# Kernel optimization log

Measured on AMD Instinct MI355X. Metric: run time of the kernel, lower is better.

Reference implementation:

```python
import jax, jax.numpy as jnp
import numpy as np

B, C, H, W = 8, 256, 128, 128
NW = 512  # n_weights (depthwise multiplier 2)
EPS = 1e-5
SPARSITY = 0.5


def setup_inputs() -> dict:
    key = jax.random.key(0)
    k_x, k_sign, k_mask, k_w1 = jax.random.split(key, 4)
    x = jax.random.normal(k_x, (B, C, H, W), dtype=jnp.float32)
    gamma = jnp.ones((C,), dtype=jnp.float32)
    beta = jnp.zeros((C,), dtype=jnp.float32)
    # frozen binary/sparse LBP depthwise weights in {-1, 0, +1}
    sign = jax.random.bernoulli(k_sign, 0.5, (NW, 1, 3, 3)).astype(jnp.float32) * 2.0 - 1.0
    inactive = jax.random.uniform(k_mask, (NW, 1, 3, 3)) > SPARSITY
    lbp_w = jnp.where(inactive, 0.0, sign)
    # 1x1 conv params (PyTorch default init scale)
    bound = 1.0 / np.sqrt(NW)
    w1 = jax.random.uniform(k_w1, (C, NW, 1, 1), minval=-bound, maxval=bound, dtype=jnp.float32)
    b1 = jnp.zeros((C,), dtype=jnp.float32)
    return {"x": x, "gamma": gamma, "beta": beta, "lbp_w": lbp_w, "w1": w1, "b1": b1}


def reference(x, gamma, beta, lbp_w, w1, b1):
    # BatchNorm2d in training mode: biased batch stats over (N, H, W)
    mean = jnp.mean(x, axis=(0, 2, 3), keepdims=True)
    var = jnp.var(x, axis=(0, 2, 3), keepdims=True)
    xn = (x - mean) * jax.lax.rsqrt(var + EPS)
    xn = xn * gamma[None, :, None, None] + beta[None, :, None, None]
    # depthwise 3x3 conv, padding=1, groups=C (depth multiplier NW//C)
    y = jax.lax.conv_general_dilated(
        xn, lbp_w, window_strides=(1, 1), padding=((1, 1), (1, 1)),
        dimension_numbers=("NCHW", "OIHW", "NCHW"), feature_group_count=C)
    y = jax.nn.relu(y)
    # 1x1 conv NW -> C plus bias, then residual add
    z = jax.lax.conv_general_dilated(
        y, w1, window_strides=(1, 1), padding=((0, 0), (0, 0)),
        dimension_numbers=("NCHW", "OIHW", "NCHW"))
    z = z + b1[None, :, None, None]
    return z + x
```

## Files before the change

### kernel.cpp

```cpp
#include <hip/hip_runtime.h>

#define B_ 8
#define C_ 256
#define H_ 128
#define W_ 128
#define NW_ 512
#define HW_ (H_*W_)
#define EPS_ 1e-5f

typedef __attribute__((ext_vector_type(8))) short bf16x8;
typedef __attribute__((ext_vector_type(4))) float f32x4;

__device__ __forceinline__ unsigned short f2bf(float f) {
  unsigned u = __float_as_uint(f);
  u += 0x7fffu + ((u >> 16) & 1u);
  return (unsigned short)(u >> 16);
}
__device__ __forceinline__ float bf2f(unsigned short h) {
  return __uint_as_float(((unsigned)h) << 16);
}
__device__ __forceinline__ float bflo(unsigned u) { return __uint_as_float(u << 16); }
__device__ __forceinline__ float bfhi(unsigned u) { return __uint_as_float(u & 0xffff0000u); }

__global__ __launch_bounds__(256)
void bn_partial(const float* __restrict__ x, float* __restrict__ psum,
                float* __restrict__ psq) {
  const int b = blockIdx.x, c = blockIdx.y, tid = threadIdx.x;
  const float4* p = (const float4*)(x + (size_t)(b*C_ + c) * HW_);
  float s = 0.f, s2 = 0.f;
  #pragma unroll
  for (int i = 0; i < 16; ++i) {
    float4 v = p[tid + i*256];
    s  += v.x + v.y + v.z + v.w;
    s2 += v.x*v.x + v.y*v.y + v.z*v.z + v.w*v.w;
  }
  #pragma unroll
  for (int off = 32; off > 0; off >>= 1) {
    s  += __shfl_down(s, off);
    s2 += __shfl_down(s2, off);
  }
  __shared__ float rs[4], rq[4];
  if ((tid & 63) == 0) { rs[tid >> 6] = s; rq[tid >> 6] = s2; }
  __syncthreads();
  if (tid == 0) {
    float S = rs[0]+rs[1]+rs[2]+rs[3], S2 = rq[0]+rq[1]+rq[2]+rq[3];
    psum[c*B_ + b] = S;
    psq [c*B_ + b] = S2;
  }
}

__global__ __launch_bounds__(256)
void bn_final(float* __restrict__ wsf, const float* __restrict__ gamma,
              const float* __restrict__ beta) {
  const int c = threadIdx.x;
  float S = 0.f, S2 = 0.f;
  #pragma unroll
  for (int b = 0; b < B_; ++b) { S += wsf[512 + c*B_ + b]; S2 += wsf[2560 + c*B_ + b]; }
  const float n = (float)(B_*HW_);
  float mean = S / n;
  float var  = S2 / n - mean*mean;
  float scl  = gamma[c] * rsqrtf(var + EPS_);
  wsf[c]       = scl;
  wsf[C_ + c]  = beta[c] - mean*scl;
}

__global__ __launch_bounds__(64)
void w1prep(const float* __restrict__ w1, ushort* __restrict__ w1f) {
  const int l15 = threadIdx.x & 15, quad = threadIdx.x >> 4;
  const int mtG = blockIdx.x >> 4, ks = blockIdx.x & 15;
  const float* src = w1 + (size_t)(mtG*16 + l15)*NW_ + ks*32 + quad*8;
  float4 f0 = *(const float4*)src, f1 = *(const float4*)(src + 4);
  union { unsigned u[4]; uint4 q; } cv;
  cv.u[0] = (unsigned)f2bf(f0.x) | ((unsigned)f2bf(f0.y) << 16);
  cv.u[1] = (unsigned)f2bf(f0.z) | ((unsigned)f2bf(f0.w) << 16);
  cv.u[2] = (unsigned)f2bf(f1.x) | ((unsigned)f2bf(f1.y) << 16);
  cv.u[3] = (unsigned)f2bf(f1.z) | ((unsigned)f2bf(f1.w) << 16);
  ((uint4*)w1f)[blockIdx.x*64 + threadIdx.x] = cv.q;
}

template<bool PREW1>
__global__ __launch_bounds__(256, 2)
void fused_mfma(const float* __restrict__ x, const float* __restrict__ lbpw,
                const float* __restrict__ w1raw, const ushort* __restrict__ w1f,
                const float* __restrict__ b1, const float* __restrict__ sc_sh,
                float* __restrict__ out) {
  const int tid  = threadIdx.x;
  const int b    = blockIdx.z;
  const int h0   = blockIdx.y * 4;
  const int w0   = blockIdx.x * 16;
  const int wave = tid >> 6;
  const int lane = tid & 63;
  const int l15  = lane & 15;
  const int quad = lane >> 4;

  __shared__ float  s_scale[C_];
  __shared__ float  s_shift[C_];
  __shared__ float  s_b1[C_];
  __shared__ __align__(16) float  s_xn[16][6][20];
  __shared__ __align__(16) ushort s_yT[64][40];
  __shared__ __align__(16) ushort s_wc[32][16];
  __shared__ __align__(16) ushort s_res[256][66];

  s_scale[tid] = sc_sh[tid];
  s_shift[tid] = sc_sh[C_ + tid];
  s_b1[tid]    = b1[tid];

  const int ccin = tid >> 4;
  const int ccol = tid & 15;

  f32x4 acc[4][4];
  #pragma unroll
  for (int mt = 0; mt < 4; ++mt)
    #pragma unroll
    for (int nt = 0; nt < 4; ++nt) {
      f32x4 z = {0.f, 0.f, 0.f, 0.f};
      acc[mt][nt] = z;
    }

  __syncthreads();

  #pragma unroll 1
  for (int kc = 0; kc < 16; ++kc) {
    const int c0 = kc * 16;
    const int o0 = kc * 32;

    for (int idx = tid; idx < 16*6*18; idx += 256) {
      const int cl  = idx / 108;
      const int rem = idx - cl * 108;
      const int r   = rem / 18;
      const int col = rem - r * 18;
      const int h = h0 + r - 1;
      const int w = w0 + col - 1;
      float v = 0.f;
      if (h >= 0 && h < H_ && w >= 0 && w < W_) {
        const float xv = x[((size_t)(b*C_ + c0 + cl)*H_ + h)*W_ + w];
        v = fmaf(xv, s_scale[c0 + cl], s_shift[c0 + cl]);
        if (r >= 1 && r <= 4 && col >= 1 && col <= 16)
          s_res[c0 + cl][(r-1)*16 + (col-1)] = f2bf(xv);
      }
      s_xn[cl][r][col] = v;
    }
    for (int idx = tid; idx < 32*9; idx += 256) {
      const int oo = idx / 9;
      const int j  = idx - oo * 9;
      s_wc[oo][j] = f2bf(lbpw[(size_t)(o0 + oo)*9 + j]);
    }
    __syncthreads();

    {
      float v[6][3];
      #pragma unroll
      for (int rr = 0; rr < 6; ++rr)
        #pragma unroll
        for (int dj = 0; dj < 3; ++dj)
          v[rr][dj] = s_xn[ccin][rr][ccol + dj];

      const uint4 qa = *(const uint4*)&s_wc[2*ccin][0];
      const uint4 qb = *(const uint4*)&s_wc[2*ccin + 1][0];
      const float wA[9] = { bflo(qa.x), bfhi(qa.x), bflo(qa.y), bfhi(qa.y),
                            bflo(qa.z), bfhi(qa.z), bflo(qa.w), bfhi(qa.w),
                            bf2f(s_wc[2*ccin][8]) };
      const float wB[9] = { bflo(qb.x), bfhi(qb.x), bflo(qb.y), bfhi(qb.y),
                            bflo(qb.z), bfhi(qb.z), bflo(qb.w), bfhi(qb.w),
                            bf2f(s_wc[2*ccin + 1][8]) };
      float a0[4] = {0.f,0.f,0.f,0.f}, a1[4] = {0.f,0.f,0.f,0.f};
      #pragma unroll
      for (int r = 0; r < 4; ++r)
        #pragma unroll
        for (int di = 0; di < 3; ++di)
          #pragma unroll
          for (int dj = 0; dj < 3; ++dj) {
            const float t = v[r + di][dj];
            a0[r] = fmaf(wA[di*3 + dj], t, a0[r]);
            a1[r] = fmaf(wB[di*3 + dj], t, a1[r]);
          }
      #pragma unroll
      for (int r = 0; r < 4; ++r) {
        const unsigned pk = (unsigned)f2bf(fmaxf(a0[r], 0.f)) |
                            ((unsigned)f2bf(fmaxf(a1[r], 0.f)) << 16);
        *(unsigned*)&s_yT[r*16 + ccol][2*ccin] = pk;
      }
    }
    __syncthreads();

    bf16x8 bfr[4];
    #pragma unroll
    for (int nt = 0; nt < 4; ++nt)
      bfr[nt] = *(const bf16x8*)&s_yT[nt*16 + l15][quad*8];

    #pragma unroll
    for (int mt = 0; mt < 4; ++mt) {
      bf16x8 afr;
      if constexpr (PREW1) {
        union { uint4 q; bf16x8 v; } cv;
        cv.q = *(const uint4*)(w1f + (size_t)(((wave*4 + mt)*16 + kc)*64 + lane)*8);
        afr = cv.v;
      } else {
        const float* wp = w1raw + (size_t)(wave*64 + mt*16 + l15)*NW_ + o0 + quad*8;
        const float4 f0 = *(const float4*)wp;
        const float4 f1 = *(const float4*)(wp + 4);
        union { unsigned u[4]; bf16x8 v; } cv;
        cv.u[0] = (unsigned)f2bf(f0.x) | ((unsigned)f2bf(f0.y) << 16);
        cv.u[1] = (unsigned)f2bf(f0.z) | ((unsigned)f2bf(f0.w) << 16);
        cv.u[2] = (unsigned)f2bf(f1.x) | ((unsigned)f2bf(f1.y) << 16);
        cv.u[3] = (unsigned)f2bf(f1.z) | ((unsigned)f2bf(f1.w) << 16);
        afr = cv.v;
      }
      #pragma unroll
      for (int nt = 0; nt < 4; ++nt)
        acc[mt][nt] = __builtin_amdgcn_mfma_f32_16x16x32_bf16(afr, bfr[nt], acc[mt][nt], 0, 0, 0);
    }
    __syncthreads();
  }

  #pragma unroll
  for (int mt = 0; mt < 4; ++mt) {
    #pragma unroll
    for (int nt = 0; nt < 4; ++nt) {
      const int h   = h0 + nt;
      const int wcl = w0 + l15;
      const int px  = nt*16 + l15;
      #pragma unroll
      for (int i = 0; i < 4; ++i) {
        const int ch = wave*64 + mt*16 + quad*4 + i;
        const float r = bf2f(s_res[ch][px]);
        out[((size_t)(b*C_ + ch)*H_ + h)*W_ + wcl] = acc[mt][nt][i] + s_b1[ch] + r;
      }
    }
  }
}

extern "C" void kernel_launch(void* const* d_in, const int* in_sizes, int n_in,
                              void* d_out, int out_size, void* d_ws, size_t ws_size,
                              hipStream_t stream) {
  const float* x     = (const float*)d_in[0];
  const float* gamma = (const float*)d_in[1];
  const float* beta  = (const float*)d_in[2];
  const float* lbpw  = (const float*)d_in[3];
  const float* w1    = (const float*)d_in[4];
  const float* b1    = (const float*)d_in[5];
  float* out = (float*)d_out;

  float* wsf = (float*)d_ws;
  ushort* w1f = (ushort*)((char*)d_ws + 18432);
  const bool pre = ws_size >= (size_t)(18432 + 262144);

  bn_partial<<<dim3(B_, C_), 256, 0, stream>>>(x, wsf + 512, wsf + 2560);
  bn_final<<<1, 256, 0, stream>>>(wsf, gamma, beta);

  dim3 grid(W_/16, H_/4, B_);
  if (pre) {
    w1prep<<<256, 64, 0, stream>>>(w1, w1f);
    fused_mfma<true><<<grid, 256, 0, stream>>>(x, lbpw, w1, w1f, b1, wsf, out);
  } else {
    fused_mfma<false><<<grid, 256, 0, stream>>>(x, lbpw, w1, w1f, b1, wsf, out);
  }
}
```

Baseline: 447.5 us.

## Double-buffer LDS staging, precompute gather geometry, drop residual LDS cache

Double-buffers the normalized input tile, LBP weights and depthwise output in LDS so the next channel chunk's gather is issued before the barrier that precedes the MFMA stage, removing one barrier per iteration. Gather addresses and padding masks are computed once per thread, and pad zeros are written once for both buffers. The residual now comes from a global re-read of x in the epilogue instead of a large bf16 LDS array, which cuts LDS use enough to request 4 blocks per SM. This also makes the residual full fp32, at the cost of extra global traffic and tighter register limits.

```diff
diff --git a/kernel.cpp b/kernel.cpp
--- a/kernel.cpp
+++ b/kernel.cpp
@@ -79,7 +79,7 @@
 }
 
 template<bool PREW1>
-__global__ __launch_bounds__(256, 2)
+__global__ __launch_bounds__(256, 4)
 void fused_mfma(const float* __restrict__ x, const float* __restrict__ lbpw,
                 const float* __restrict__ w1raw, const ushort* __restrict__ w1f,
                 const float* __restrict__ b1, const float* __restrict__ sc_sh,
@@ -92,60 +92,75 @@
   const int lane = tid & 63;
   const int l15  = lane & 15;
   const int quad = lane >> 4;
+  const int cl   = tid >> 4;
+  const int jj   = tid & 15;
 
   __shared__ float  s_scale[C_];
   __shared__ float  s_shift[C_];
   __shared__ float  s_b1[C_];
-  __shared__ __align__(16) float  s_xn[16][6][20];
-  __shared__ __align__(16) ushort s_yT[64][40];
-  __shared__ __align__(16) ushort s_wc[32][16];
-  __shared__ __align__(16) ushort s_res[256][66];
+  __shared__ __align__(16) float  s_xn[2][16][6][20];
+  __shared__ __align__(16) ushort s_yT[2][64][40];
+  __shared__ __align__(16) ushort s_wc[2][32][16];
 
   s_scale[tid] = sc_sh[tid];
   s_shift[tid] = sc_sh[C_ + tid];
   s_b1[tid]    = b1[tid];
 
-  const int ccin = tid >> 4;
-  const int ccol = tid & 15;
-
-  f32x4 acc[4][4];
-  #pragma unroll
-  for (int mt = 0; mt < 4; ++mt)
-    #pragma unroll
-    for (int nt = 0; nt < 4; ++nt) {
-      f32x4 z = {0.f, 0.f, 0.f, 0.f};
-      acc[mt][nt] = z;
-    }
-
-  __syncthreads();
-
-  #pragma unroll 1
-  for (int kc = 0; kc < 16; ++kc) {
-    const int c0 = kc * 16;
-    const int o0 = kc * 32;
-
-    for (int idx = tid; idx < 16*6*18; idx += 256) {
-      const int cl  = idx / 108;
-      const int rem = idx - cl * 108;
-      const int r   = rem / 18;
-      const int col = rem - r * 18;
+  int geo[7];
+  unsigned actmask = 0, padmask = 0;
+  #pragma unroll
+  for (int k = 0; k < 7; ++k) {
+    geo[k] = 0;
+    const int e = jj + 16*k;
+    if (e < 108) {
+      const int r   = e / 18;
+      const int col = e - r*18;
+      const int lofs = cl*120 + r*20 + col;
       const int h = h0 + r - 1;
       const int w = w0 + col - 1;
-      float v = 0.f;
       if (h >= 0 && h < H_ && w >= 0 && w < W_) {
-        const float xv = x[((size_t)(b*C_ + c0 + cl)*H_ + h)*W_ + w];
-        v = fmaf(xv, s_scale[c0 + cl], s_shift[c0 + cl]);
-        if (r >= 1 && r <= 4 && col >= 1 && col <= 16)
-          s_res[c0 + cl][(r-1)*16 + (col-1)] = f2bf(xv);
-      }
-      s_xn[cl][r][col] = v;
-    }
-    for (int idx = tid; idx < 32*9; idx += 256) {
-      const int oo = idx / 9;
-      const int j  = idx - oo * 9;
-      s_wc[oo][j] = f2bf(lbpw[(size_t)(o0 + oo)*9 + j]);
-    }
-    __syncthreads();
+        actmask |= (1u << k);
+        geo[k] = ((cl*HW_ + h*W_ + w) << 11) | lofs;
+      } else {
+        padmask |= (1u << k);
+        geo[k] = lofs;
+      }
+    }
+  }
+  {
+    float* p0 = &s_xn[0][0][0][0];
+    float* p1 = &s_xn[1][0][0][0];
+    #pragma unroll
+    for (int k = 0; k < 7; ++k)
+      if (padmask & (1u << k)) { p0[geo[k] & 2047] = 0.f; p1[geo[k] & 2047] = 0.f; }
+  }
+  const int woA = tid / 9,         wjA = tid - woA*9;
+  const int woB = (tid + 256) / 9, wjB = (tid + 256) - woB*9;
+
+  f32x4 acc[4][4];
+  #pragma unroll
+  for (int mt = 0; mt < 4; ++mt)
+    #pragma unroll
+    for (int nt = 0; nt < 4; ++nt) { f32x4 z = {0.f,0.f,0.f,0.f}; acc[mt][nt] = z; }
+
+  __syncthreads();
+
+  {
+    const float scl = s_scale[cl];
+    const float sh  = s_shift[cl];
+    const float* xc = x + (size_t)(b*C_) * HW_;
+    float* xb = &s_xn[0][0][0][0];
+    #pragma unroll
+    for (int k = 0; k < 7; ++k)
+      if (actmask & (1u << k)) xb[geo[k] & 2047] = fmaf(xc[geo[k] >> 11], scl, sh);
+    s_wc[0][woA][wjA] = f2bf(lbpw[woA*9 + wjA]);
+    if (tid < 32) s_wc[0][woB][wjB] = f2bf(lbpw[woB*9 + wjB]);
+  }
+  __syncthreads();
+
+  #pragma unroll 2
+  for (int kc = 0; kc < 16; ++kc) {
+    const int p = kc & 1;
 
     {
       float v[6][3];
@@ -153,16 +168,16 @@
       for (int rr = 0; rr < 6; ++rr)
         #pragma unroll
         for (int dj = 0; dj < 3; ++dj)
-          v[rr][dj] = s_xn[ccin][rr][ccol + dj];
-
-      const uint4 qa = *(const uint4*)&s_wc[2*ccin][0];
-      const uint4 qb = *(const uint4*)&s_wc[2*ccin + 1][0];
+          v[rr][dj] = s_xn[p][cl][rr][jj + dj];
+
+      const uint4 qa = *(const uint4*)&s_wc[p][2*cl][0];
+      const uint4 qb = *(const uint4*)&s_wc[p][2*cl + 1][0];
       const float wA[9] = { bflo(qa.x), bfhi(qa.x), bflo(qa.y), bfhi(qa.y),
                             bflo(qa.z), bfhi(qa.z), bflo(qa.w), bfhi(qa.w),
-                            bf2f(s_wc[2*ccin][8]) };
+                            bf2f(s_wc[p][2*cl][8]) };
       const float wB[9] = { bflo(qb.x), bfhi(qb.x), bflo(qb.y), bfhi(qb.y),
                             bflo(qb.z), bfhi(qb.z), bflo(qb.w), bfhi(qb.w),
-                            bf2f(s_wc[2*ccin + 1][8]) };
+                            bf2f(s_wc[p][2*cl + 1][8]) };
       float a0[4] = {0.f,0.f,0.f,0.f}, a1[4] = {0.f,0.f,0.f,0.f};
       #pragma unroll
       for (int r = 0; r < 4; ++r)
@@ -178,15 +193,30 @@
       for (int r = 0; r < 4; ++r) {
         const unsigned pk = (unsigned)f2bf(fmaxf(a0[r], 0.f)) |
                             ((unsigned)f2bf(fmaxf(a1[r], 0.f)) << 16);
-        *(unsigned*)&s_yT[r*16 + ccol][2*ccin] = pk;
-      }
-    }
+        *(unsigned*)&s_yT[p][r*16 + jj][2*cl] = pk;
+      }
+    }
+
+    if (kc < 15) {
+      const int c0 = (kc + 1) * 16;
+      const float scl = s_scale[c0 + cl];
+      const float sh  = s_shift[c0 + cl];
+      const float* xc = x + (size_t)(b*C_ + c0) * HW_;
+      float* xb = &s_xn[p ^ 1][0][0][0];
+      #pragma unroll
+      for (int k = 0; k < 7; ++k)
+        if (actmask & (1u << k)) xb[geo[k] & 2047] = fmaf(xc[geo[k] >> 11], scl, sh);
+      const int o0 = (kc + 1) * 32;
+      s_wc[p ^ 1][woA][wjA] = f2bf(lbpw[(o0 + woA)*9 + wjA]);
+      if (tid < 32) s_wc[p ^ 1][woB][wjB] = f2bf(lbpw[(o0 + woB)*9 + wjB]);
+    }
+
     __syncthreads();
 
     bf16x8 bfr[4];
     #pragma unroll
     for (int nt = 0; nt < 4; ++nt)
-      bfr[nt] = *(const bf16x8*)&s_yT[nt*16 + l15][quad*8];
+      bfr[nt] = *(const bf16x8*)&s_yT[p][nt*16 + l15][quad*8];
 
     #pragma unroll
     for (int mt = 0; mt < 4; ++mt) {
@@ -196,7 +226,7 @@
         cv.q = *(const uint4*)(w1f + (size_t)(((wave*4 + mt)*16 + kc)*64 + lane)*8);
         afr = cv.v;
       } else {
-        const float* wp = w1raw + (size_t)(wave*64 + mt*16 + l15)*NW_ + o0 + quad*8;
+        const float* wp = w1raw + (size_t)(wave*64 + mt*16 + l15)*NW_ + kc*32 + quad*8;
         const float4 f0 = *(const float4*)wp;
         const float4 f1 = *(const float4*)(wp + 4);
         union { unsigned u[4]; bf16x8 v; } cv;
@@ -210,21 +240,18 @@
       for (int nt = 0; nt < 4; ++nt)
         acc[mt][nt] = __builtin_amdgcn_mfma_f32_16x16x32_bf16(afr, bfr[nt], acc[mt][nt], 0, 0, 0);
     }
-    __syncthreads();
   }
 
   #pragma unroll
   for (int mt = 0; mt < 4; ++mt) {
     #pragma unroll
     for (int nt = 0; nt < 4; ++nt) {
-      const int h   = h0 + nt;
-      const int wcl = w0 + l15;
-      const int px  = nt*16 + l15;
+      const int h = h0 + nt;
       #pragma unroll
       for (int i = 0; i < 4; ++i) {
         const int ch = wave*64 + mt*16 + quad*4 + i;
-        const float r = bf2f(s_res[ch][px]);
-        out[((size_t)(b*C_ + ch)*H_ + h)*W_ + wcl] = acc[mt][nt][i] + s_b1[ch] + r;
+        const size_t o = ((size_t)(b*C_ + ch)*H_ + h)*W_ + (w0 + l15);
+        out[o] = acc[mt][nt][i] + s_b1[ch] + x[o];
       }
     }
   }
```

Result: faster. 415.9 us (-7.1%).

## Restructure fused kernel: per-wave rows, register-prefetched double-buffered input, no block barriers

Applied to the files above, without the earlier changes.

Each wave now owns one output row and computes every output channel (16 M-tiles), so the depthwise result feeds the MFMA B operand straight from registers without the shared transpose buffer. Input tiles are staged per wave in a double-buffered shared buffer, and the next channel group's global loads are issued into registers before the current compute, which removes the per-iteration __syncthreads. Depthwise weights are preloaded once, bias seeds the accumulators, and the residual is re-read from global x in the epilogue instead of a bf16 shared copy. The occupancy hint rises to 3 blocks per SM. The cost is more accumulator registers (64 floats), reloading the full w1 per wave, and halo rows fetched redundantly across waves.

```diff
diff --git a/kernel.cpp b/kernel.cpp
--- a/kernel.cpp
+++ b/kernel.cpp
@@ -15,9 +15,6 @@
   unsigned u = __float_as_uint(f);
   u += 0x7fffu + ((u >> 16) & 1u);
   return (unsigned short)(u >> 16);
-}
-__device__ __forceinline__ float bf2f(unsigned short h) {
-  return __uint_as_float(((unsigned)h) << 16);
 }
 __device__ __forceinline__ float bflo(unsigned u) { return __uint_as_float(u << 16); }
 __device__ __forceinline__ float bfhi(unsigned u) { return __uint_as_float(u & 0xffff0000u); }
@@ -79,7 +76,7 @@
 }
 
 template<bool PREW1>
-__global__ __launch_bounds__(256, 2)
+__global__ __launch_bounds__(256, 3)
 void fused_mfma(const float* __restrict__ x, const float* __restrict__ lbpw,
                 const float* __restrict__ w1raw, const ushort* __restrict__ w1f,
                 const float* __restrict__ b1, const float* __restrict__ sc_sh,
@@ -88,115 +85,154 @@
   const int b    = blockIdx.z;
   const int h0   = blockIdx.y * 4;
   const int w0   = blockIdx.x * 16;
-  const int wave = tid >> 6;
+  const int wv   = tid >> 6;
   const int lane = tid & 63;
   const int l15  = lane & 15;
   const int quad = lane >> 4;
 
   __shared__ float  s_scale[C_];
   __shared__ float  s_shift[C_];
-  __shared__ float  s_b1[C_];
-  __shared__ __align__(16) float  s_xn[16][6][20];
-  __shared__ __align__(16) ushort s_yT[64][40];
-  __shared__ __align__(16) ushort s_wc[32][16];
-  __shared__ __align__(16) ushort s_res[256][66];
+  __shared__ __align__(16) float  s_xn[2][4][1216];
+  __shared__ __align__(16) ushort s_wp[256][24];
 
   s_scale[tid] = sc_sh[tid];
   s_shift[tid] = sc_sh[C_ + tid];
-  s_b1[tid]    = b1[tid];
-
-  const int ccin = tid >> 4;
-  const int ccol = tid & 15;
-
-  f32x4 acc[4][4];
-  #pragma unroll
-  for (int mt = 0; mt < 4; ++mt)
-    #pragma unroll
-    for (int nt = 0; nt < 4; ++nt) {
-      f32x4 z = {0.f, 0.f, 0.f, 0.f};
-      acc[mt][nt] = z;
-    }
+  {
+    const float* wp0 = lbpw + (size_t)(2*tid)*9;
+    #pragma unroll
+    for (int t = 0; t < 9; ++t) {
+      s_wp[tid][2*t]   = f2bf(wp0[t]);
+      s_wp[tid][2*t+1] = f2bf(wp0[9 + t]);
+    }
+  }
+
+  const int hbase = h0 + wv - 1;
+  int gI[3], lI[3], cIdx[3]; unsigned mI = 0;
+  #pragma unroll
+  for (int k = 0; k < 3; ++k) {
+    const int slot = lane + 64*k;
+    const int ch = slot / 12;
+    const int rem = slot - ch*12;
+    const int r = rem >> 2, q = rem & 3;
+    cIdx[k] = ch;
+    lI[k] = ch*76 + r*24 + 4 + q*4;
+    const int h = hbase + r;
+    gI[k] = ch*HW_ + h*W_ + w0 + q*4;
+    if (h >= 0 && h < H_) mI |= (1u << k);
+  }
+  int gH[2], lH[2], cHx[2]; unsigned mH = 0, eH = 0;
+  #pragma unroll
+  for (int k = 0; k < 2; ++k) {
+    const int slot = lane + 64*k;
+    gH[k] = 0; lH[k] = 0; cHx[k] = 0;
+    if (slot < 96) {
+      eH |= (1u << k);
+      const int ch = slot / 6;
+      const int rem = slot - ch*6;
+      const int r = rem >> 1, side = rem & 1;
+      cHx[k] = ch;
+      lH[k] = ch*76 + r*24 + (side ? 20 : 3);
+      const int h = hbase + r;
+      const int w = w0 + (side ? 16 : -1);
+      gH[k] = ch*HW_ + h*W_ + w;
+      if (h >= 0 && h < H_ && w >= 0 && w < W_) mH |= (1u << k);
+    }
+  }
+  {
+    float* s0 = &s_xn[0][wv][0];
+    float* s1 = &s_xn[1][wv][0];
+    const float4 z4 = {0.f, 0.f, 0.f, 0.f};
+    #pragma unroll
+    for (int k = 0; k < 3; ++k)
+      if (!(mI & (1u << k))) { *(float4*)(s0 + lI[k]) = z4; *(float4*)(s1 + lI[k]) = z4; }
+    #pragma unroll
+    for (int k = 0; k < 2; ++k)
+      if ((eH & (1u << k)) && !(mH & (1u << k))) { s0[lH[k]] = 0.f; s1[lH[k]] = 0.f; }
+  }
+
+  f32x4 acc[16];
+  #pragma unroll
+  for (int mt = 0; mt < 16; ++mt)
+    acc[mt] = *(const f32x4*)(b1 + mt*16 + quad*4);
 
   __syncthreads();
 
-  #pragma unroll 1
+  {
+    const float* xc = x + (size_t)(b*C_) * HW_;
+    float* sb = &s_xn[0][wv][0];
+    #pragma unroll
+    for (int k = 0; k < 3; ++k) if (mI & (1u << k)) {
+      const float4 t = *(const float4*)(xc + gI[k]);
+      const float sc = s_scale[cIdx[k]], sh = s_shift[cIdx[k]];
+      float4 o; o.x = fmaf(t.x, sc, sh); o.y = fmaf(t.y, sc, sh);
+                o.z = fmaf(t.z, sc, sh); o.w = fmaf(t.w, sc, sh);
+      *(float4*)(sb + lI[k]) = o;
+    }
+    #pragma unroll
+    for (int k = 0; k < 2; ++k) if (mH & (1u << k))
+      sb[lH[k]] = fmaf(xc[gH[k]], s_scale[cHx[k]], s_shift[cHx[k]]);
+  }
+
+  #pragma unroll 2
   for (int kc = 0; kc < 16; ++kc) {
-    const int c0 = kc * 16;
-    const int o0 = kc * 32;
-
-    for (int idx = tid; idx < 16*6*18; idx += 256) {
-      const int cl  = idx / 108;
-      const int rem = idx - cl * 108;
-      const int r   = rem / 18;
-      const int col = rem - r * 18;
-      const int h = h0 + r - 1;
-      const int w = w0 + col - 1;
-      float v = 0.f;
-      if (h >= 0 && h < H_ && w >= 0 && w < W_) {
-        const float xv = x[((size_t)(b*C_ + c0 + cl)*H_ + h)*W_ + w];
-        v = fmaf(xv, s_scale[c0 + cl], s_shift[c0 + cl]);
-        if (r >= 1 && r <= 4 && col >= 1 && col <= 16)
-          s_res[c0 + cl][(r-1)*16 + (col-1)] = f2bf(xv);
-      }
-      s_xn[cl][r][col] = v;
-    }
-    for (int idx = tid; idx < 32*9; idx += 256) {
-      const int oo = idx / 9;
-      const int j  = idx - oo * 9;
-      s_wc[oo][j] = f2bf(lbpw[(size_t)(o0 + oo)*9 + j]);
-    }
-    __syncthreads();
-
+    const int p = kc & 1;
+
+    float4 rA0 = {0,0,0,0}, rA1 = {0,0,0,0}, rA2 = {0,0,0,0};
+    float rH0 = 0.f, rH1 = 0.f;
+    if (kc < 15) {
+      const float* xc = x + (size_t)(b*C_ + (kc+1)*16) * HW_;
+      if (mI & 1u) rA0 = *(const float4*)(xc + gI[0]);
+      if (mI & 2u) rA1 = *(const float4*)(xc + gI[1]);
+      if (mI & 4u) rA2 = *(const float4*)(xc + gI[2]);
+      if (mH & 1u) rH0 = xc[gH[0]];
+      if (mH & 2u) rH1 = xc[gH[1]];
+    }
+
+    float a[8];
+    #pragma unroll
+    for (int j = 0; j < 8; ++j) a[j] = 0.f;
     {
-      float v[6][3];
+      const float* sb = &s_xn[p][wv][0];
       #pragma unroll
-      for (int rr = 0; rr < 6; ++rr)
-        #pragma unroll
-        for (int dj = 0; dj < 3; ++dj)
-          v[rr][dj] = s_xn[ccin][rr][ccol + dj];
-
-      const uint4 qa = *(const uint4*)&s_wc[2*ccin][0];
-      const uint4 qb = *(const uint4*)&s_wc[2*ccin + 1][0];
-      const float wA[9] = { bflo(qa.x), bfhi(qa.x), bflo(qa.y), bfhi(qa.y),
-                            bflo(qa.z), bfhi(qa.z), bflo(qa.w), bfhi(qa.w),
-                            bf2f(s_wc[2*ccin][8]) };
-      const float wB[9] = { bflo(qb.x), bfhi(qb.x), bflo(qb.y), bfhi(qb.y),
-                            bflo(qb.z), bfhi(qb.z), bflo(qb.w), bfhi(qb.w),
-                            bf2f(s_wc[2*ccin + 1][8]) };
-      float a0[4] = {0.f,0.f,0.f,0.f}, a1[4] = {0.f,0.f,0.f,0.f};
-      #pragma unroll
-      for (int r = 0; r < 4; ++r)
+      for (int ci = 0; ci < 4; ++ci) {
+        const int cin = quad*4 + ci;
+        const ushort* wr = &s_wp[kc*16 + cin][0];
+        const uint4 wq  = *(const uint4*)(wr);
+        const uint4 wq2 = *(const uint4*)(wr + 8);
+        const unsigned w8 = *(const unsigned*)(wr + 16);
+        const unsigned wtap[9] = { wq.x, wq.y, wq.z, wq.w,
+                                   wq2.x, wq2.y, wq2.z, wq2.w, w8 };
+        const float* xb = sb + cin*76 + 3 + l15;
+        float a0 = 0.f, a1 = 0.f;
         #pragma unroll
         for (int di = 0; di < 3; ++di)
           #pragma unroll
           for (int dj = 0; dj < 3; ++dj) {
-            const float t = v[r + di][dj];
-            a0[r] = fmaf(wA[di*3 + dj], t, a0[r]);
-            a1[r] = fmaf(wB[di*3 + dj], t, a1[r]);
+            const unsigned wd = wtap[di*3 + dj];
+            const float v = xb[di*24 + dj];
+            a0 = fmaf(bflo(wd), v, a0);
+            a1 = fmaf(bfhi(wd), v, a1);
           }
-      #pragma unroll
-      for (int r = 0; r < 4; ++r) {
-        const unsigned pk = (unsigned)f2bf(fmaxf(a0[r], 0.f)) |
-                            ((unsigned)f2bf(fmaxf(a1[r], 0.f)) << 16);
-        *(unsigned*)&s_yT[r*16 + ccol][2*ccin] = pk;
-      }
-    }
-    __syncthreads();
-
-    bf16x8 bfr[4];
-    #pragma unroll
-    for (int nt = 0; nt < 4; ++nt)
-      bfr[nt] = *(const bf16x8*)&s_yT[nt*16 + l15][quad*8];
-
-    #pragma unroll
-    for (int mt = 0; mt < 4; ++mt) {
+        a[2*ci]   = a0;
+        a[2*ci+1] = a1;
+      }
+    }
+    union { unsigned u[4]; bf16x8 v; } yv;
+    #pragma unroll
+    for (int t = 0; t < 4; ++t)
+      yv.u[t] = (unsigned)f2bf(fmaxf(a[2*t], 0.f)) |
+                ((unsigned)f2bf(fmaxf(a[2*t+1], 0.f)) << 16);
+    const bf16x8 bfr = yv.v;
+
+    #pragma unroll
+    for (int mt = 0; mt < 16; ++mt) {
       bf16x8 afr;
       if constexpr (PREW1) {
         union { uint4 q; bf16x8 v; } cv;
-        cv.q = *(const uint4*)(w1f + (size_t)(((wave*4 + mt)*16 + kc)*64 + lane)*8);
+        cv.q = *(const uint4*)(w1f + (size_t)((mt*16 + kc)*64 + lane)*8);
         afr = cv.v;
       } else {
-        const float* wp = w1raw + (size_t)(wave*64 + mt*16 + l15)*NW_ + o0 + quad*8;
+        const float* wp = w1raw + (size_t)(mt*16 + l15)*NW_ + kc*32 + quad*8;
         const float4 f0 = *(const float4*)wp;
         const float4 f1 = *(const float4*)(wp + 4);
         union { unsigned u[4]; bf16x8 v; } cv;
@@ -206,26 +242,43 @@
         cv.u[3] = (unsigned)f2bf(f1.z) | ((unsigned)f2bf(f1.w) << 16);
         afr = cv.v;
       }
-      #pragma unroll
-      for (int nt = 0; nt < 4; ++nt)
-        acc[mt][nt] = __builtin_amdgcn_mfma_f32_16x16x32_bf16(afr, bfr[nt], acc[mt][nt], 0, 0, 0);
-    }
-    __syncthreads();
-  }
-
-  #pragma unroll
-  for (int mt = 0; mt < 4; ++mt) {
-    #pragma unroll
-    for (int nt = 0; nt < 4; ++nt) {
-      const int h   = h0 + nt;
-      const int wcl = w0 + l15;
-      const int px  = nt*16 + l15;
-      #pragma unroll
-      for (int i = 0; i < 4; ++i) {
-        const int ch = wave*64 + mt*16 + quad*4 + i;
-        const float r = bf2f(s_res[ch][px]);
-        out[((size_t)(b*C_ + ch)*H_ + h)*W_ + wcl] = acc[mt][nt][i] + s_b1[ch] + r;
-      }
+      acc[mt] = __builtin_amdgcn_mfma_f32_16x16x32_bf16(afr, bfr, acc[mt], 0, 0, 0);
+    }
+
+    if (kc < 15) {
+      const int c1 = (kc + 1) * 16;
+      float* sb = &s_xn[p ^ 1][wv][0];
+      if (mI & 1u) {
+        const float sc = s_scale[c1 + cIdx[0]], sh = s_shift[c1 + cIdx[0]];
+        float4 o; o.x = fmaf(rA0.x, sc, sh); o.y = fmaf(rA0.y, sc, sh);
+                  o.z = fmaf(rA0.z, sc, sh); o.w = fmaf(rA0.w, sc, sh);
+        *(float4*)(sb + lI[0]) = o;
+      }
+      if (mI & 2u) {
+        const float sc = s_scale[c1 + cIdx[1]], sh = s_shift[c1 + cIdx[1]];
+        float4 o; o.x = fmaf(rA1.x, sc, sh); o.y = fmaf(rA1.y, sc, sh);
+                  o.z = fmaf(rA1.z, sc, sh); o.w = fmaf(rA1.w, sc, sh);
+        *(float4*)(sb + lI[1]) = o;
+      }
+      if (mI & 4u) {
+        const float sc = s_scale[c1 + cIdx[2]], sh = s_shift[c1 + cIdx[2]];
+        float4 o; o.x = fmaf(rA2.x, sc, sh); o.y = fmaf(rA2.y, sc, sh);
+                  o.z = fmaf(rA2.z, sc, sh); o.w = fmaf(rA2.w, sc, sh);
+        *(float4*)(sb + lI[2]) = o;
+      }
+      if (mH & 1u) sb[lH[0]] = fmaf(rH0, s_scale[c1 + cHx[0]], s_shift[c1 + cHx[0]]);
+      if (mH & 2u) sb[lH[1]] = fmaf(rH1, s_scale[c1 + cHx[1]], s_shift[c1 + cHx[1]]);
+    }
+  }
+
+  const int hrow = h0 + wv;
+  #pragma unroll
+  for (int mt = 0; mt < 16; ++mt) {
+    #pragma unroll
+    for (int i = 0; i < 4; ++i) {
+      const int ch = mt*16 + quad*4 + i;
+      const size_t o = ((size_t)(b*C_ + ch)*H_ + hrow)*W_ + (w0 + l15);
+      out[o] = acc[mt][i] + x[o];
     }
   }
 }
```

Result: slower. 509.2 us (+13.8%).
